# Kernel tuning notes

Measured on AMD Instinct MI355X. Metric: run time of the kernel, lower is better.

## Reference

```python
import jax, jax.numpy as jnp
import numpy as np

B, S, D = 128, 144, 1024  # batch, grid tokens (12x12), d_model
GRID = 12


def _relative_position(grid_size):
    # Reconstructs get_grids_pos for a grid_size x grid_size grid of unit cells
    # (x_min = cell col/row index, x_max = x_min + 1), standard grid-feature layout.
    x = jnp.arange(grid_size, dtype=jnp.float32)
    px_min = jnp.repeat(x, grid_size)          # (S,) varies slowly (rows)
    py_min = jnp.tile(x, grid_size)            # (S,) varies fast (cols)
    px_max = px_min + 1.0
    py_max = py_min + 1.0
    cx = (px_min + px_max) * 0.5
    cy = (py_min + py_max) * 0.5
    w = px_max - px_min + 1.0                  # == 2 everywhere
    h = py_max - py_min + 1.0
    eps = 1e-10
    dx = jnp.log(jnp.maximum(jnp.abs((cx[:, None] - cx[None, :]) / w[:, None]), eps))
    dy = jnp.log(jnp.maximum(jnp.abs((cy[:, None] - cy[None, :]) / h[:, None]), eps))
    dw = jnp.log(w[:, None] / w[None, :])
    dh = jnp.log(h[:, None] / h[None, :])
    return jnp.stack([dx, dy, dw, dh], axis=-1)  # (S, S, 4)


def setup_inputs() -> dict:
    key = jax.random.key(0)
    ks = jax.random.split(key, 12)
    std = 0.02
    return {
        "query": jax.random.normal(ks[0], (B, S, D), jnp.float32),
        "key":   jax.random.normal(ks[1], (B, S, D), jnp.float32),
        "value": jax.random.normal(ks[2], (B, S, D), jnp.float32),
        # Linear weights stored as (in, out): y = x @ W + b
        "Wq": jax.random.normal(ks[3], (D, D), jnp.float32) * std,
        "bq": jnp.zeros((D,), jnp.float32),
        "Wk": jax.random.normal(ks[4], (D, D), jnp.float32) * std,
        "bk": jnp.zeros((D,), jnp.float32),
        "Wv": jax.random.normal(ks[5], (D, D), jnp.float32) * std,
        "bv": jnp.zeros((D,), jnp.float32),
        "Wl": jax.random.normal(ks[6], (4, D), jnp.float32) * std,
        "bl": jnp.zeros((D,), jnp.float32),
        "w_g": jax.random.normal(ks[7], (S, D, 1), jnp.float32) * std,
    }


def reference(query, key, value, Wq, bq, Wk, bk, Wv, bv, Wl, bl, w_g):
    d_model = query.shape[-1]
    scale = d_model ** (-0.5)
    act = jax.nn.relu  # get_activation_function() assumed relu; dropout=0 (eval)

    q = act(query @ Wq + bq)   # (B,S,D)
    k = act(key @ Wk + bk)
    v = act(value @ Wv + bv)

    attn = jnp.einsum('bid,bjd->bij', q, k) * scale  # (B,S,S)

    seq = value.shape[1]
    pos = _relative_position(int(round(seq ** 0.5)))  # (S,S,4)
    rel = act(pos @ Wl + bl)                          # (S,S,D)
    # torch.matmul(rela_pos, w_g): row i of the grid uses w_g[i]
    bias = act(jnp.einsum('ijd,id->ij', rel, w_g[..., 0]))  # (S,S)

    attn = jax.nn.softmax(attn + bias[None, :, :], axis=-1)
    return jnp.einsum('bij,bjd->bid', attn, v)
```

## Files before the change

### kernel.cpp

```cpp
#include <hip/hip_runtime.h>
#include <hip/hip_bf16.h>
#include <stdint.h>

#define SS 144
#define DD 1024
#define NB 128
#define SP 160
#define SCALE 0.03125f

typedef __attribute__((ext_vector_type(8))) short short8;
typedef __attribute__((ext_vector_type(4))) float floatx4;
typedef unsigned short u16;

#define MFMA(a, b, c) __builtin_amdgcn_mfma_f32_16x16x32_bf16((a), (b), (c), 0, 0, 0)

__device__ __forceinline__ u16 f2bf(float f) {
    union { float f; unsigned int i; } v; v.f = f;
    unsigned int r = v.i + 0x7fff + ((v.i >> 16) & 1);
    return (u16)(r >> 16);
}
__device__ __forceinline__ short8 pack8(float4 a, float4 b) {
    short8 r;
    r[0] = (short)f2bf(a.x); r[1] = (short)f2bf(a.y);
    r[2] = (short)f2bf(a.z); r[3] = (short)f2bf(a.w);
    r[4] = (short)f2bf(b.x); r[5] = (short)f2bf(b.y);
    r[6] = (short)f2bf(b.z); r[7] = (short)f2bf(b.w);
    return r;
}

__global__ void transpose_w_k(const float* __restrict__ Wq, const float* __restrict__ Wk,
                              const float* __restrict__ Wv, u16* __restrict__ WT) {
    __shared__ u16 t[32][33];
    int z = blockIdx.z;
    const float* W = z == 0 ? Wq : (z == 1 ? Wk : Wv);
    u16* O = WT + (size_t)z * DD * DD;
    int bn = blockIdx.x * 32, bk = blockIdx.y * 32;
    int tx = threadIdx.x & 31, ty = threadIdx.x >> 5;
    for (int r = ty; r < 32; r += 8) t[r][tx] = f2bf(W[(size_t)(bk + r) * DD + bn + tx]);
    __syncthreads();
    for (int r = ty; r < 32; r += 8) O[(size_t)(bn + r) * DD + bk + tx] = t[tx][r];
}

__global__ void bias_k(const float* __restrict__ Wl, const float* __restrict__ bl,
                       const float* __restrict__ wg, float* __restrict__ biasb) {
    int ij = blockIdx.x;
    int i = ij / SS, j = ij - i * SS;
    int lane = threadIdx.x;
    int ri = i / 12, ci = i - ri * 12, rj = j / 12, cj = j - rj * 12;
    float dx = logf(fmaxf(fabsf((float)(ri - rj)) * 0.5f, 1e-10f));
    float dy = logf(fmaxf(fabsf((float)(ci - cj)) * 0.5f, 1e-10f));
    float s = 0.f;
    for (int d = lane; d < DD; d += 64) {
        float r = dx * Wl[d] + dy * Wl[DD + d] + bl[d];
        r = fmaxf(r, 0.f);
        s += r * wg[(size_t)i * DD + d];
    }
    #pragma unroll
    for (int m = 32; m > 0; m >>= 1) s += __shfl_xor(s, m);
    if (lane == 0) biasb[ij] = fmaxf(s, 0.f);
}

__global__ __launch_bounds__(256) void proj_k(
    const float* __restrict__ Xq, const float* __restrict__ Xk, const float* __restrict__ Xv,
    const u16* __restrict__ WT,
    const float* __restrict__ bq, const float* __restrict__ bk, const float* __restrict__ bv,
    u16* __restrict__ Oq, u16* __restrict__ Ok, u16* __restrict__ OvT) {
    __shared__ __align__(16) u16 As[128 * 32];
    __shared__ __align__(16) u16 Bs[128 * 32];
    int z = blockIdx.z;
    const float* X = z == 0 ? Xq : (z == 1 ? Xk : Xv);
    const u16* Wt = WT + (size_t)z * DD * DD;
    const float* bias = z == 0 ? bq : (z == 1 ? bk : bv);
    int bm = blockIdx.x, bn = blockIdx.y;
    int tid = threadIdx.x, lane = tid & 63, wv = tid >> 6;
    int wm = wv >> 1, wn = wv & 1;
    int lr = lane & 15, lq = lane >> 4;

    floatx4 zero4 = {0.f, 0.f, 0.f, 0.f};
    floatx4 acc[4][4];
    #pragma unroll
    for (int r = 0; r < 4; r++)
        #pragma unroll
        for (int c = 0; c < 4; c++) acc[r][c] = zero4;

    const float* Xbase = X + (size_t)bm * 128 * DD;
    const u16* Wbase = Wt + (size_t)bn * 128 * DD;

    int c0 = tid, c1 = tid + 256;
    int row0 = c0 >> 2, ko0 = (c0 & 3) << 3;
    int row1 = c1 >> 2, ko1 = (c1 & 3) << 3;

    for (int k0 = 0; k0 < DD; k0 += 32) {
        const float* p0 = Xbase + (size_t)row0 * DD + k0 + ko0;
        const float* p1 = Xbase + (size_t)row1 * DD + k0 + ko1;
        float4 a0 = *(const float4*)p0, a0b = *(const float4*)(p0 + 4);
        float4 a1 = *(const float4*)p1, a1b = *(const float4*)(p1 + 4);
        short8 xb0 = *(const short8*)(Wbase + (size_t)row0 * DD + k0 + ko0);
        short8 xb1 = *(const short8*)(Wbase + (size_t)row1 * DD + k0 + ko1);
        short8 xa0 = pack8(a0, a0b);
        short8 xa1 = pack8(a1, a1b);
        __syncthreads();
        *(short8*)&As[c0 * 8] = xa0;
        *(short8*)&As[c1 * 8] = xa1;
        *(short8*)&Bs[c0 * 8] = xb0;
        *(short8*)&Bs[c1 * 8] = xb1;
        __syncthreads();
        short8 a[4], b[4];
        #pragma unroll
        for (int r = 0; r < 4; r++)
            a[r] = *(const short8*)&As[(wm * 64 + r * 16 + lr) * 32 + lq * 8];
        #pragma unroll
        for (int c = 0; c < 4; c++)
            b[c] = *(const short8*)&Bs[(wn * 64 + c * 16 + lr) * 32 + lq * 8];
        #pragma unroll
        for (int r = 0; r < 4; r++)
            #pragma unroll
            for (int c = 0; c < 4; c++)
                acc[r][c] = MFMA(a[r], b[c], acc[r][c]);
    }

    int mrow0 = bm * 128 + wm * 64;
    int ncol0 = bn * 128 + wn * 64;
    if (z < 2) {
        u16* O = z == 0 ? Oq : Ok;
        #pragma unroll
        for (int r = 0; r < 4; r++)
            #pragma unroll
            for (int c = 0; c < 4; c++) {
                int col = ncol0 + c * 16 + lr;
                float bb = bias[col];
                #pragma unroll
                for (int i = 0; i < 4; i++) {
                    int row = mrow0 + r * 16 + lq * 4 + i;
                    O[(size_t)row * DD + col] = f2bf(fmaxf(acc[r][c][i] + bb, 0.f));
                }
            }
    } else {
        #pragma unroll
        for (int r = 0; r < 4; r++)
            #pragma unroll
            for (int c = 0; c < 4; c++) {
                int col = ncol0 + c * 16 + lr;
                float bb = bias[col];
                #pragma unroll
                for (int i = 0; i < 4; i++) {
                    int row = mrow0 + r * 16 + lq * 4 + i;
                    int bidx = row / SS;
                    int srow = row - bidx * SS;
                    OvT[((size_t)bidx * DD + col) * SP + srow] =
                        f2bf(fmaxf(acc[r][c][i] + bb, 0.f));
                }
            }
    }
}

__global__ __launch_bounds__(256) void attn_k(
    const u16* __restrict__ q, const u16* __restrict__ k,
    const float* __restrict__ biasb, u16* __restrict__ probs) {
    __shared__ float Sst[16][148];
    int it = blockIdx.x, b = blockIdx.y;
    int i0 = it * 16;
    int tid = threadIdx.x, lane = tid & 63, wv = tid >> 6;
    int lr = lane & 15, lq = lane >> 4;
    const u16* qs = q + ((size_t)b * SS + i0) * DD;
    const u16* ks = k + (size_t)b * SS * DD;

    floatx4 zero4 = {0.f, 0.f, 0.f, 0.f};
    floatx4 acc[3] = {zero4, zero4, zero4};
    int nt = (wv == 0) ? 3 : 2;

    for (int d0 = 0; d0 < DD; d0 += 32) {
        short8 a = *(const short8*)&qs[(size_t)lr * DD + d0 + lq * 8];
        #pragma unroll
        for (int m = 0; m < 3; m++) {
            if (m < nt) {
                int t = wv + m * 4;
                short8 bb = *(const short8*)&ks[(size_t)(t * 16 + lr) * DD + d0 + lq * 8];
                acc[m] = MFMA(a, bb, acc[m]);
            }
        }
    }
    for (int m = 0; m < nt; m++) {
        int t = wv + m * 4;
        #pragma unroll
        for (int i = 0; i < 4; i++) {
            int row = lq * 4 + i, col = t * 16 + lr;
            Sst[row][col] = acc[m][i] * SCALE + biasb[(i0 + row) * SS + col];
        }
    }
    __syncthreads();

    int g = tid >> 4, j = tid & 15;
    float mx = -1e30f;
    for (int c = j; c < SS; c += 16) mx = fmaxf(mx, Sst[g][c]);
    #pragma unroll
    for (int m = 1; m < 16; m <<= 1) mx = fmaxf(mx, __shfl_xor(mx, m));
    float sm = 0.f;
    float ev[9];
    int t = 0;
    for (int c = j; c < SS; c += 16, t++) { float e = expf(Sst[g][c] - mx); ev[t] = e; sm += e; }
    #pragma unroll
    for (int m = 1; m < 16; m <<= 1) sm += __shfl_xor(sm, m);
    float inv = 1.f / sm;
    u16* pr = probs + ((size_t)b * SS + i0 + g) * SP;
    t = 0;
    for (int c = j; c < SP; c += 16, t++) {
        float val = (c < SS) ? ev[t < 9 ? t : 8] * inv : 0.f;
        pr[c] = f2bf(val);
    }
}

__global__ __launch_bounds__(256) void pv_k(
    const u16* __restrict__ probs, const u16* __restrict__ vT, float* __restrict__ out) {
    int cb = blockIdx.x, it = blockIdx.y, b = blockIdx.z;
    int tid = threadIdx.x, lane = tid & 63, wv = tid >> 6;
    int lr = lane & 15, lq = lane >> 4;
    const u16* pr = probs + ((size_t)b * SS + it * 16) * SP;
    const u16* vt = vT + (size_t)b * DD * SP;
    int col0 = cb * 256 + wv * 64;

    floatx4 zero4 = {0.f, 0.f, 0.f, 0.f};
    floatx4 acc[4] = {zero4, zero4, zero4, zero4};
    for (int k0 = 0; k0 < SP; k0 += 32) {
        short8 a = *(const short8*)&pr[(size_t)lr * SP + k0 + lq * 8];
        #pragma unroll
        for (int c = 0; c < 4; c++) {
            short8 bb = *(const short8*)&vt[(size_t)(col0 + c * 16 + lr) * SP + k0 + lq * 8];
            acc[c] = MFMA(a, bb, acc[c]);
        }
    }
    #pragma unroll
    for (int c = 0; c < 4; c++)
        #pragma unroll
        for (int i = 0; i < 4; i++) {
            int row = it * 16 + lq * 4 + i, col = col0 + c * 16 + lr;
            out[((size_t)b * SS + row) * DD + col] = acc[c][i];
        }
}

extern "C" void kernel_launch(void* const* d_in, const int* in_sizes, int n_in,
                              void* d_out, int out_size, void* d_ws, size_t ws_size,
                              hipStream_t stream) {
    const float* query = (const float*)d_in[0];
    const float* key_  = (const float*)d_in[1];
    const float* value = (const float*)d_in[2];
    const float* Wq = (const float*)d_in[3];
    const float* bq = (const float*)d_in[4];
    const float* Wk = (const float*)d_in[5];
    const float* bk = (const float*)d_in[6];
    const float* Wv = (const float*)d_in[7];
    const float* bv = (const float*)d_in[8];
    const float* Wl = (const float*)d_in[9];
    const float* bl = (const float*)d_in[10];
    const float* wg = (const float*)d_in[11];

    u16* WT    = (u16*)d_ws;
    u16* q     = WT + (size_t)3 * DD * DD;
    u16* k     = q  + (size_t)NB * SS * DD;
    u16* vT    = k  + (size_t)NB * SS * DD;
    u16* probs = vT + (size_t)NB * DD * SP;
    float* biasb = (float*)(probs + (size_t)NB * SS * SP);

    transpose_w_k<<<dim3(32, 32, 3), 256, 0, stream>>>(Wq, Wk, Wv, WT);
    bias_k<<<dim3(SS * SS), 64, 0, stream>>>(Wl, bl, wg, biasb);
    proj_k<<<dim3(144, 8, 3), 256, 0, stream>>>(query, key_, value, WT,
                                                bq, bk, bv, q, k, vT);
    attn_k<<<dim3(9, NB), 256, 0, stream>>>(q, k, biasb, probs);
    pv_k<<<dim3(4, 9, NB), 256, 0, stream>>>(probs, vT, (float*)d_out);
}
```

Measured before the change: 655.1 us.

## Pre-convert activations to bf16 and stage GEMM tiles via direct global-to-LDS loads

Adds a separate conversion pass that casts each input activation tensor to bf16 in a shared workspace buffer. The projection GEMM then loads both operand tiles with global_load_lds, skipping the register round trip and the in-loop fp32 packing. The three projections now run as sequential conversion and GEMM launch pairs instead of one launch over three z-slices. The extra conversion pass reads and writes the activations once more and adds launches, but the GEMM re-reads the activations eight times (once per N tile), so halving those bytes may pay for it.

```diff
diff --git a/kernel.cpp b/kernel.cpp
--- a/kernel.cpp
+++ b/kernel.cpp
@@ -26,6 +26,22 @@
     r[4] = (short)f2bf(b.x); r[5] = (short)f2bf(b.y);
     r[6] = (short)f2bf(b.z); r[7] = (short)f2bf(b.w);
     return r;
+}
+
+__device__ __forceinline__ void gload16(u16* lds, const u16* g) {
+    __builtin_amdgcn_global_load_lds(
+        (__attribute__((address_space(1))) void*)g,
+        (__attribute__((address_space(3))) void*)lds, 16, 0, 0);
+}
+
+__global__ __launch_bounds__(256) void convert_k(const float* __restrict__ X,
+                                                 u16* __restrict__ O, int nchunk) {
+    for (int c = blockIdx.x * 256 + threadIdx.x; c < nchunk; c += gridDim.x * 256) {
+        size_t i = (size_t)c * 8;
+        float4 a = *(const float4*)(X + i);
+        float4 b = *(const float4*)(X + i + 4);
+        *(short8*)(O + i) = pack8(a, b);
+    }
 }
 
 __global__ void transpose_w_k(const float* __restrict__ Wq, const float* __restrict__ Wk,
@@ -61,16 +77,11 @@
 }
 
 __global__ __launch_bounds__(256) void proj_k(
-    const float* __restrict__ Xq, const float* __restrict__ Xk, const float* __restrict__ Xv,
-    const u16* __restrict__ WT,
-    const float* __restrict__ bq, const float* __restrict__ bk, const float* __restrict__ bv,
-    u16* __restrict__ Oq, u16* __restrict__ Ok, u16* __restrict__ OvT) {
+    const u16* __restrict__ Xb, const u16* __restrict__ Wt,
+    const float* __restrict__ bias,
+    u16* __restrict__ O, u16* __restrict__ OvT, int z) {
     __shared__ __align__(16) u16 As[128 * 32];
     __shared__ __align__(16) u16 Bs[128 * 32];
-    int z = blockIdx.z;
-    const float* X = z == 0 ? Xq : (z == 1 ? Xk : Xv);
-    const u16* Wt = WT + (size_t)z * DD * DD;
-    const float* bias = z == 0 ? bq : (z == 1 ? bk : bv);
     int bm = blockIdx.x, bn = blockIdx.y;
     int tid = threadIdx.x, lane = tid & 63, wv = tid >> 6;
     int wm = wv >> 1, wn = wv & 1;
@@ -83,27 +94,25 @@
         #pragma unroll
         for (int c = 0; c < 4; c++) acc[r][c] = zero4;
 
-    const float* Xbase = X + (size_t)bm * 128 * DD;
-    const u16* Wbase = Wt + (size_t)bn * 128 * DD;
+    const u16* Abase = Xb + (size_t)bm * 128 * DD;
+    const u16* Bbase = Wt + (size_t)bn * 128 * DD;
 
     int c0 = tid, c1 = tid + 256;
-    int row0 = c0 >> 2, ko0 = (c0 & 3) << 3;
-    int row1 = c1 >> 2, ko1 = (c1 & 3) << 3;
+    const u16* ga0 = Abase + (size_t)(c0 >> 2) * DD + ((c0 & 3) << 3);
+    const u16* ga1 = Abase + (size_t)(c1 >> 2) * DD + ((c1 & 3) << 3);
+    const u16* gb0 = Bbase + (size_t)(c0 >> 2) * DD + ((c0 & 3) << 3);
+    const u16* gb1 = Bbase + (size_t)(c1 >> 2) * DD + ((c1 & 3) << 3);
+    u16* la0 = &As[c0 * 8];
+    u16* la1 = &As[c1 * 8];
+    u16* lb0 = &Bs[c0 * 8];
+    u16* lb1 = &Bs[c1 * 8];
 
     for (int k0 = 0; k0 < DD; k0 += 32) {
-        const float* p0 = Xbase + (size_t)row0 * DD + k0 + ko0;
-        const float* p1 = Xbase + (size_t)row1 * DD + k0 + ko1;
-        float4 a0 = *(const float4*)p0, a0b = *(const float4*)(p0 + 4);
-        float4 a1 = *(const float4*)p1, a1b = *(const float4*)(p1 + 4);
-        short8 xb0 = *(const short8*)(Wbase + (size_t)row0 * DD + k0 + ko0);
-        short8 xb1 = *(const short8*)(Wbase + (size_t)row1 * DD + k0 + ko1);
-        short8 xa0 = pack8(a0, a0b);
-        short8 xa1 = pack8(a1, a1b);
         __syncthreads();
-        *(short8*)&As[c0 * 8] = xa0;
-        *(short8*)&As[c1 * 8] = xa1;
-        *(short8*)&Bs[c0 * 8] = xb0;
-        *(short8*)&Bs[c1 * 8] = xb1;
+        gload16(la0, ga0 + k0);
+        gload16(la1, ga1 + k0);
+        gload16(lb0, gb0 + k0);
+        gload16(lb1, gb1 + k0);
         __syncthreads();
         short8 a[4], b[4];
         #pragma unroll
@@ -122,7 +131,6 @@
     int mrow0 = bm * 128 + wm * 64;
     int ncol0 = bn * 128 + wn * 64;
     if (z < 2) {
-        u16* O = z == 0 ? Oq : Ok;
         #pragma unroll
         for (int r = 0; r < 4; r++)
             #pragma unroll
@@ -255,7 +263,8 @@
     const float* wg = (const float*)d_in[11];
 
     u16* WT    = (u16*)d_ws;
-    u16* q     = WT + (size_t)3 * DD * DD;
+    u16* Xbf   = WT + (size_t)3 * DD * DD;
+    u16* q     = Xbf + (size_t)NB * SS * DD;
     u16* k     = q  + (size_t)NB * SS * DD;
     u16* vT    = k  + (size_t)NB * SS * DD;
     u16* probs = vT + (size_t)NB * DD * SP;
@@ -263,8 +272,15 @@
 
     transpose_w_k<<<dim3(32, 32, 3), 256, 0, stream>>>(Wq, Wk, Wv, WT);
     bias_k<<<dim3(SS * SS), 64, 0, stream>>>(Wl, bl, wg, biasb);
-    proj_k<<<dim3(144, 8, 3), 256, 0, stream>>>(query, key_, value, WT,
-                                                bq, bk, bv, q, k, vT);
+
+    const float* Xs[3] = {query, key_, value};
+    const float* bs[3] = {bq, bk, bv};
+    int nchunk = NB * SS * DD / 8;
+    for (int z = 0; z < 3; z++) {
+        convert_k<<<dim3(2048), 256, 0, stream>>>(Xs[z], Xbf, nchunk);
+        proj_k<<<dim3(144, 8), 256, 0, stream>>>(Xbf, WT + (size_t)z * DD * DD, bs[z],
+                                                 z == 0 ? q : k, vT, z);
+    }
     attn_k<<<dim3(9, NB), 256, 0, stream>>>(q, k, biasb, probs);
     pv_k<<<dim3(4, 9, NB), 256, 0, stream>>>(probs, vT, (float*)d_out);
 }
```

New measurement: 646.6 us. About the same (-1.3%).
